# Kernel optimization log

Hardware: AMD Instinct MI355X
Metric: run time of the kernel (lower is better)

Reference implementation:

```python
import jax, jax.numpy as jnp
import numpy as np

B, N, D, H, DH = 4, 1024, 1024, 16, 64
INNER = H * DH  # 1024


def setup_inputs() -> dict:
    key = jax.random.key(0)
    k0, k1, k2, k3 = jax.random.split(key, 4)
    x = jax.random.normal(k0, (B, N, D), dtype=jnp.float32)
    # float 0/1 padding mask per token
    mask = jax.random.randint(k1, (B, N), 0, 2).astype(jnp.float32)
    w_qkv = jax.random.normal(k2, (D, 3 * INNER), dtype=jnp.float32) * (D ** -0.5)
    w_out = jax.random.normal(k3, (INNER, D), dtype=jnp.float32) * (INNER ** -0.5)
    b_out = jnp.zeros((D,), dtype=jnp.float32)
    return {"x": x, "mask": mask, "w_qkv": w_qkv, "w_out": w_out, "b_out": b_out}


def reference(x, mask, w_qkv, w_out, b_out):
    scale = DH ** -0.5
    qkv = x @ w_qkv  # [B,N,3*INNER]
    q, k, v = jnp.split(qkv, 3, axis=-1)
    resh = lambda t: t.reshape(B, N, H, DH).transpose(0, 2, 1, 3)  # b h n d
    q, k, v = resh(q), resh(k), resh(v)
    dots = jnp.einsum('bhnd,bhmd->bhnm', q, k) * scale  # [B,H,N,N]
    # attn_bias = 1 - m_i*m_j; blocked where isclose(attn_bias, 1) i.e. pair ~ 0
    pair = mask[:, None, :, None] * mask[:, None, None, :]  # [B,1,N,N]
    blocked = jnp.isclose(1.0 - pair, jnp.ones_like(pair))
    dots = jnp.where(blocked, -jnp.inf, dots)
    # fully-masked-row fixup: rows that are all -inf get dots=0, attn forced to 0
    valid = jnp.any(dots != -jnp.inf, axis=-1, keepdims=True)  # [B,H,N,1]
    dots = jnp.where(valid, dots, 0.0)
    attn = jax.nn.softmax(dots, axis=-1)
    attn = jnp.where(valid, attn, 0.0)
    out = jnp.einsum('bhnm,bhmd->bhnd', attn, v)
    out = out.transpose(0, 2, 1, 3).reshape(B, N, INNER)
    return out @ w_out + b_out
```

## Files before the change

kernel.cpp:

```cpp
#include <hip/hip_runtime.h>

#define INF __builtin_inff()

typedef __attribute__((ext_vector_type(8))) short bf16x8;
typedef __attribute__((ext_vector_type(4))) short s16x4;
typedef __attribute__((ext_vector_type(4))) float f32x4;
typedef __attribute__((ext_vector_type(8))) unsigned short u16x8;
typedef __attribute__((ext_vector_type(4))) unsigned short u16x4;

#define MFMA16(a, b, c) __builtin_amdgcn_mfma_f32_16x16x32_bf16(a, b, c, 0, 0, 0)

#define ASYNC16(g, l) __builtin_amdgcn_global_load_lds( \
    (const __attribute__((address_space(1))) unsigned int*)(const void*)(g), \
    (__attribute__((address_space(3))) unsigned int*)(void*)(l), 16, 0, 0)

__device__ __forceinline__ unsigned short f2bf(float f) {
  union { float f; unsigned u; } v; v.f = f;
  unsigned r = v.u + 0x7fffu + ((v.u >> 16) & 1u);
  return (unsigned short)(r >> 16);
}

__global__ __launch_bounds__(1024) void k_scan(
    const float* __restrict__ mask, unsigned short* __restrict__ perm, int* __restrict__ nv) {
  __shared__ int wsum[16];
  __shared__ int woff[16];
  const int b = blockIdx.x, t = threadIdx.x;
  const int wid = t >> 6, lane = t & 63;
  const bool valid = (mask[b * 1024 + t] != 0.f);
  unsigned long long bal = __ballot(valid);
  int pre = __popcll(bal & ((1ull << lane) - 1ull));
  if (lane == 0) wsum[wid] = __popcll(bal);
  __syncthreads();
  if (t < 16) { int s = 0; for (int i = 0; i < t; ++i) s += wsum[i]; woff[t] = s; }
  __syncthreads();
  int p = woff[wid] + pre;
  if (valid) perm[b * 1024 + p] = (unsigned short)t;
  if (t == 1023) nv[b] = woff[15] + wsum[15];
}

__global__ __launch_bounds__(256) void k_cvtg(
    const float* __restrict__ x, const unsigned short* __restrict__ perm,
    const int* __restrict__ nvb, unsigned short* __restrict__ xc) {
  const int id = blockIdx.x;
  const int b = id >> 10, slot = id & 1023;
  const int nv = nvb[b];
  const int ce = (nv + 127) & ~127;
  if (slot >= ce) return;
  const int t = threadIdx.x;
  u16x4 o;
  if (slot < nv) {
    int tok = perm[b * 1024 + slot];
    float4 f = ((const float4*)(x + ((size_t)(b * 1024 + tok)) * 1024))[t];
    o[0] = f2bf(f.x); o[1] = f2bf(f.y); o[2] = f2bf(f.z); o[3] = f2bf(f.w);
  } else {
    o[0] = o[1] = o[2] = o[3] = 0;
  }
  ((u16x4*)(xc + ((size_t)(b * 1024 + slot)) * 1024))[t] = o;
}

__global__ __launch_bounds__(256) void k_transpose_cvt(
    const float* __restrict__ src, unsigned short* __restrict__ dst, int R, int C) {
  __shared__ float tile[32][33];
  int bc = blockIdx.x * 32;
  int br = blockIdx.y * 32;
  int tx = threadIdx.x & 31, ty = threadIdx.x >> 5;
#pragma unroll
  for (int i = 0; i < 32; i += 8)
    tile[ty + i][tx] = src[(size_t)(br + ty + i) * C + bc + tx];
  __syncthreads();
#pragma unroll
  for (int i = 0; i < 32; i += 8)
    dst[(size_t)(bc + ty + i) * R + br + tx] = f2bf(tile[tx][ty + i]);
}

__global__ __launch_bounds__(256) void k_gemm_qkv(
    const unsigned short* __restrict__ A, const unsigned short* __restrict__ Bt,
    const int* __restrict__ nvb,
    unsigned short* __restrict__ qcmp, unsigned short* __restrict__ kcmp,
    unsigned short* __restrict__ vcmp) {
  __shared__ unsigned short SH[16384];
  unsigned short* As = SH;
  unsigned short* Bs = SH + 8192;
  const int lid = blockIdx.x;
  const int xcd = lid & 7, i6 = lid >> 3;
  const int colt = xcd * 3 + (i6 % 3);
  const int rowt = i6 / 3;
  const int b = rowt >> 3, mt = rowt & 7;
  const int nv = nvb[b];
  if (mt * 128 >= nv) return;
  const int bm0 = mt * 128;
  const int bn0 = colt * 128;
  const size_t abase = ((size_t)(b * 1024 + bm0)) * 1024;
  const int t = threadIdx.x;
  const int lane = t & 63, wave = t >> 6;
  const int wm = (wave >> 1) * 64, wn = (wave & 1) * 64;
  const int lr = lane & 15, quad = lane >> 4;
  const int sw = lr & 7;
  f32x4 acc[4][4] = {};
  for (int k0 = 0; k0 < 1024; k0 += 64) {
    __syncthreads();
#pragma unroll
    for (int j = 0; j < 4; ++j) {
      int idx = t + j * 256;
      int row = idx >> 3;
      int g = (idx ^ row) & 7;
      ASYNC16(&A[abase + (size_t)row * 1024 + k0 + g * 8], &As[idx * 8]);
      ASYNC16(&Bt[((size_t)(bn0 + row)) * 1024 + k0 + g * 8], &Bs[idx * 8]);
    }
    __syncthreads();
#pragma unroll
    for (int ks = 0; ks < 2; ++ks) {
      bf16x8 af[4], bfr[4];
#pragma unroll
      for (int i = 0; i < 4; ++i)
        af[i] = *(const bf16x8*)(&As[(wm + i * 16 + lr) * 64 + (((ks * 4 + quad) ^ sw)) * 8]);
#pragma unroll
      for (int j = 0; j < 4; ++j)
        bfr[j] = *(const bf16x8*)(&Bs[(wn + j * 16 + lr) * 64 + (((ks * 4 + quad) ^ sw)) * 8]);
#pragma unroll
      for (int i = 0; i < 4; ++i)
#pragma unroll
        for (int j = 0; j < 4; ++j)
          acc[i][j] = MFMA16(af[i], bfr[j], acc[i][j]);
    }
  }
  const int sec = bn0 >> 10;
  unsigned short* dstT = (sec == 0) ? qcmp : (sec == 1) ? kcmp : vcmp;
  const int js0 = bn0 & 1023;
#pragma unroll
  for (int hh = 0; hh < 2; ++hh) {
    __syncthreads();
    if ((wave >> 1) == hh) {
#pragma unroll
      for (int i = 0; i < 4; ++i)
#pragma unroll
        for (int j = 0; j < 4; ++j)
#pragma unroll
          for (int r = 0; r < 4; ++r)
            SH[(i * 16 + quad * 4 + r) * 136 + wn + j * 16 + lr] = f2bf(acc[i][j][r]);
    }
    __syncthreads();
#pragma unroll
    for (int rr = 0; rr < 4; ++rr) {
      int lrow = (t >> 4) + rr * 16;
      int ck = t & 15;
      int slot = bm0 + hh * 64 + lrow;
      int js = js0 + ck * 8;
      int h = js >> 6, d = js & 63;
      u16x8 v = *(u16x8*)(&SH[lrow * 136 + ck * 8]);
      *(u16x8*)(&dstT[(((size_t)(b * 16 + h)) * 1024 + slot) * 64 + d]) = v;
    }
  }
}

__global__ __launch_bounds__(256) void k_vtrans(
    const unsigned short* __restrict__ vc, unsigned short* __restrict__ vt,
    const int* __restrict__ nvb) {
  __shared__ unsigned short tile[32][33];
  const int bh = blockIdx.z;
  const int s0 = blockIdx.y * 32;
  const int d0 = blockIdx.x * 32;
  const int nv = nvb[bh >> 4];
  if (s0 >= ((nv + 63) & ~63)) return;
  const int tx = threadIdx.x & 31, ty = threadIdx.x >> 5;
  const unsigned short* src = vc + ((size_t)bh << 16);
  unsigned short* dst = vt + ((size_t)bh << 16);
#pragma unroll
  for (int i = 0; i < 32; i += 8)
    tile[ty + i][tx] = src[(size_t)(s0 + ty + i) * 64 + d0 + tx];
  __syncthreads();
#pragma unroll
  for (int i = 0; i < 32; i += 8) {
    int slot = s0 + tx;
    dst[(size_t)(d0 + ty + i) * 1024 + slot] = (slot < nv) ? tile[tx][ty + i] : (unsigned short)0;
  }
}

__global__ __launch_bounds__(256) void k_padzero(
    unsigned short* __restrict__ aoc, const int* __restrict__ nvb) {
  const int b = blockIdx.x;
  const int nv = nvb[b];
  const int ce = (nv + 63) & ~63;
  for (int r = nv; r < ce; ++r)
    ((unsigned long long*)(aoc + ((size_t)(b * 1024 + r)) * 1024))[threadIdx.x] = 0ull;
}

__global__ __launch_bounds__(256, 4) void k_attn(
    const unsigned short* __restrict__ qcmp, const unsigned short* __restrict__ kcmp,
    const unsigned short* __restrict__ vtc, const int* __restrict__ nvb,
    unsigned short* __restrict__ aoc) {
  __shared__ unsigned short Ks[64 * 64];
  __shared__ unsigned short Vs[64 * 64];
  __shared__ unsigned short P[4][16 * 72];
  const int bx = blockIdx.x;
  const int bh = (bx & 7) + 8 * (bx >> 7);
  const int qcb = (bx >> 3) & 15;
  const int b = bh >> 4, h = bh & 15;
  const int nv = nvb[b];
  if (qcb * 64 >= nv) return;
  const int t = threadIdx.x;
  const int wave = t >> 6, lane = t & 63;
  const int lr = lane & 15, quad = lane >> 4;
  const int q0 = qcb * 64 + wave * 16;
  const unsigned short* qp = qcmp + ((size_t)bh << 16);
  const unsigned short* kp = kcmp + ((size_t)bh << 16);
  const unsigned short* vp = vtc + ((size_t)bh << 16);
  unsigned short* Pw = P[wave];
  bf16x8 qv0 = *(const bf16x8*)(qp + (q0 + lr) * 64 + quad * 8);
  bf16x8 qv1 = *(const bf16x8*)(qp + (q0 + lr) * 64 + 32 + quad * 8);
  float m = -INF, l = 0.f;
  f32x4 o[4] = {};
  const int sw = lr & 7;
  const int nk = (nv + 63) >> 6;
  for (int it = 0; it < nk; ++it) {
    const int kc0 = it * 64;
    __syncthreads();
#pragma unroll
    for (int ld = 0; ld < 2; ++ld) {
      int idx = t + ld * 256;
      int row = idx >> 3;
      int gch = (idx ^ row) & 7;
      ASYNC16(kp + (kc0 + row) * 64 + gch * 8, &Ks[idx * 8]);
      ASYNC16(vp + (size_t)row * 1024 + kc0 + gch * 8, &Vs[idx * 8]);
    }
    __syncthreads();
    f32x4 st[4];
#pragma unroll
    for (int tt = 0; tt < 4; ++tt) {
      int krow = tt * 16 + lr;
      bf16x8 k0 = *(const bf16x8*)(&Ks[krow * 64 + ((quad ^ sw)) * 8]);
      bf16x8 k1 = *(const bf16x8*)(&Ks[krow * 64 + (((4 + quad) ^ sw)) * 8]);
      f32x4 c = {};
      c = MFMA16(k0, qv0, c);
      c = MFMA16(k1, qv1, c);
      st[tt] = c;
    }
    float tm = -INF;
#pragma unroll
    for (int tt = 0; tt < 4; ++tt) {
#pragma unroll
      for (int r = 0; r < 4; ++r) {
        int slot = kc0 + tt * 16 + quad * 4 + r;
        float v = (slot < nv) ? st[tt][r] * 0.125f : -INF;
        st[tt][r] = v;
        tm = fmaxf(tm, v);
      }
    }
    tm = fmaxf(tm, __shfl_xor(tm, 16));
    tm = fmaxf(tm, __shfl_xor(tm, 32));
    float mn = fmaxf(m, tm);
    float alpha = __expf(m - mn);
    if (m == -INF) alpha = 1.f;
    float ps = 0.f;
#pragma unroll
    for (int tt = 0; tt < 4; ++tt) {
      s16x4 pv;
#pragma unroll
      for (int r = 0; r < 4; ++r) {
        float pe = __expf(st[tt][r] - mn);
        ps += pe;
        pv[r] = (short)f2bf(pe);
      }
      *(s16x4*)(&Pw[lr * 72 + tt * 16 + quad * 4]) = pv;
    }
    ps += __shfl_xor(ps, 16);
    ps += __shfl_xor(ps, 32);
    l = l * alpha + ps;
    m = mn;
    float ar[4];
#pragma unroll
    for (int r = 0; r < 4; ++r) ar[r] = __shfl(alpha, quad * 4 + r);
#pragma unroll
    for (int jj = 0; jj < 4; ++jj)
#pragma unroll
      for (int r = 0; r < 4; ++r) o[jj][r] *= ar[r];
#pragma unroll
    for (int sh = 0; sh < 2; ++sh) {
      bf16x8 pa = *(const bf16x8*)(&Pw[lr * 72 + sh * 32 + quad * 8]);
#pragma unroll
      for (int jj = 0; jj < 4; ++jj) {
        bf16x8 vbf = *(const bf16x8*)(&Vs[(jj * 16 + lr) * 64 + (((sh * 4 + quad) ^ sw)) * 8]);
        o[jj] = MFMA16(pa, vbf, o[jj]);
      }
    }
  }
  float inv = 1.f / l;
  float ir[4];
#pragma unroll
  for (int r = 0; r < 4; ++r) ir[r] = __shfl(inv, quad * 4 + r);
#pragma unroll
  for (int r = 0; r < 4; ++r) {
    int slot = q0 + quad * 4 + r;
    if (slot < nv) {
      size_t rowb = ((size_t)(b * 1024 + slot)) * 1024 + h * 64;
#pragma unroll
      for (int jj = 0; jj < 4; ++jj)
        aoc[rowb + jj * 16 + lr] = f2bf(o[jj][r] * ir[r]);
    }
  }
}

__global__ __launch_bounds__(256) void k_biasfill(
    const float* __restrict__ bias, float* __restrict__ out) {
  int idx = blockIdx.x * 256 + threadIdx.x;
  int row = idx >> 8, c4 = idx & 255;
  ((float4*)out)[(size_t)row * 256 + c4] = ((const float4*)bias)[c4];
}

__global__ __launch_bounds__(256) void k_gemm_out(
    const unsigned short* __restrict__ A, const unsigned short* __restrict__ Bt,
    const unsigned short* __restrict__ perm, const int* __restrict__ nvb,
    const float* __restrict__ bias, float* __restrict__ C) {
  __shared__ unsigned short SH[12288];
  unsigned short* As = SH;
  unsigned short* Bs = SH + 4096;
  const int lid = blockIdx.x;
  const int col = lid & 7;
  const int rt = lid >> 3;
  const int b = rt >> 4, mt = rt & 15;
  const int nv = nvb[b];
  if (mt * 64 >= nv) return;
  const int bm0 = mt * 64;
  const int bn0 = col * 128;
  const size_t abase = ((size_t)(b * 1024 + bm0)) * 1024;
  const int t = threadIdx.x;
  const int lane = t & 63, wave = t >> 6;
  const int wm = (wave >> 1) * 32, wn = (wave & 1) * 64;
  const int lr = lane & 15, quad = lane >> 4;
  const int sw = lr & 7;
  f32x4 acc[2][4] = {};
  for (int k0 = 0; k0 < 1024; k0 += 64) {
    __syncthreads();
#pragma unroll
    for (int j = 0; j < 2; ++j) {
      int idx = t + j * 256;
      int row = idx >> 3;
      int g = (idx ^ row) & 7;
      ASYNC16(&A[abase + (size_t)row * 1024 + k0 + g * 8], &As[idx * 8]);
    }
#pragma unroll
    for (int j = 0; j < 4; ++j) {
      int idx = t + j * 256;
      int row = idx >> 3;
      int g = (idx ^ row) & 7;
      ASYNC16(&Bt[((size_t)(bn0 + row)) * 1024 + k0 + g * 8], &Bs[idx * 8]);
    }
    __syncthreads();
#pragma unroll
    for (int ks = 0; ks < 2; ++ks) {
      bf16x8 af[2], bfr[4];
#pragma unroll
      for (int i = 0; i < 2; ++i)
        af[i] = *(const bf16x8*)(&As[(wm + i * 16 + lr) * 64 + (((ks * 4 + quad) ^ sw)) * 8]);
#pragma unroll
      for (int j = 0; j < 4; ++j)
        bfr[j] = *(const bf16x8*)(&Bs[(wn + j * 16 + lr) * 64 + (((ks * 4 + quad) ^ sw)) * 8]);
#pragma unroll
      for (int i = 0; i < 2; ++i)
#pragma unroll
        for (int j = 0; j < 4; ++j)
          acc[i][j] = MFMA16(af[i], bfr[j], acc[i][j]);
    }
  }
#pragma unroll
  for (int i = 0; i < 2; ++i)
#pragma unroll
    for (int r = 0; r < 4; ++r) {
      int slot = bm0 + wm + i * 16 + quad * 4 + r;
      if (slot < nv) {
        int tok = perm[b * 1024 + slot];
        size_t rowb = ((size_t)(b * 1024 + tok)) * 1024;
#pragma unroll
        for (int j = 0; j < 4; ++j) {
          int c = bn0 + wn + j * 16 + lr;
          C[rowb + c] = acc[i][j][r] + bias[c];
        }
      }
    }
}

extern "C" void kernel_launch(void* const* d_in, const int* in_sizes, int n_in,
                              void* d_out, int out_size, void* d_ws, size_t ws_size,
                              hipStream_t stream) {
  const float* x    = (const float*)d_in[0];
  const float* mask = (const float*)d_in[1];
  const float* wqkv = (const float*)d_in[2];
  const float* wout = (const float*)d_in[3];
  const float* bout = (const float*)d_in[4];
  float* out = (float*)d_out;
  char* ws = (char*)d_ws;
  unsigned short* xc    = (unsigned short*)(ws);
  unsigned short* vtc   = (unsigned short*)(ws);
  unsigned short* wqkvt = (unsigned short*)(ws + (size_t)( 8 << 20));
  unsigned short* woutt = (unsigned short*)(ws + (size_t)(14 << 20));
  unsigned short* qcmp  = (unsigned short*)(ws + (size_t)(16 << 20));
  unsigned short* kcmp  = (unsigned short*)(ws + (size_t)(24 << 20));
  unsigned short* vcmp  = (unsigned short*)(ws + (size_t)(32 << 20));
  unsigned short* aoc   = (unsigned short*)(ws + (size_t)(32 << 20));
  unsigned short* perm  = (unsigned short*)(ws + (size_t)(40 << 20));
  int*            nvb   = (int*)           (ws + (size_t)(40 << 20) + 8192);

  k_scan<<<4, 1024, 0, stream>>>(mask, perm, nvb);
  k_cvtg<<<4096, 256, 0, stream>>>(x, perm, nvb, xc);
  k_transpose_cvt<<<dim3(96, 32), 256, 0, stream>>>(wqkv, wqkvt, 1024, 3072);
  k_transpose_cvt<<<dim3(32, 32), 256, 0, stream>>>(wout, woutt, 1024, 1024);
  k_gemm_qkv<<<768, 256, 0, stream>>>(xc, wqkvt, nvb, qcmp, kcmp, vcmp);
  k_vtrans<<<dim3(2, 32, 64), 256, 0, stream>>>(vcmp, vtc, nvb);
  k_padzero<<<4, 256, 0, stream>>>(aoc, nvb);
  k_attn<<<1024, 256, 0, stream>>>(qcmp, kcmp, vtc, nvb, aoc);
  k_biasfill<<<4096, 256, 0, stream>>>(bout, out);
  k_gemm_out<<<512, 256, 0, stream>>>(aoc, woutt, perm, nvb, bout, out);
}
```

Baseline: 165.0 us.

## Double-buffer GEMM/attention loads, fuse V transpose, merge and trim auxiliary kernels

Adds two-stage LDS double buffering to the QKV GEMM, the attention K/V loads and the output GEMM, so the next tile's async global-to-LDS copy is issued while the current tile is computed. The V output is now written directly in transposed layout from the QKV GEMM epilogue, which removes the separate V-transpose kernel. The two weight-transpose launches are merged into one. The attention output buffer now aliases the zero-padded xc buffer, which removes the pad-zeroing kernel. The scan also records masked tokens in perm, so the bias fill writes only masked rows instead of the whole output. Doubling the shared memory lowers attention occupancy (launch bounds go from 4 to 3 blocks) and raises LDS pressure in the GEMMs.

```diff
diff --git a/kernel.cpp b/kernel.cpp
--- a/kernel.cpp
+++ b/kernel.cpp
@@ -33,9 +33,10 @@
   __syncthreads();
   if (t < 16) { int s = 0; for (int i = 0; i < t; ++i) s += wsum[i]; woff[t] = s; }
   __syncthreads();
-  int p = woff[wid] + pre;
-  if (valid) perm[b * 1024 + p] = (unsigned short)t;
-  if (t == 1023) nv[b] = woff[15] + wsum[15];
+  const int nvt = woff[15] + wsum[15];
+  const int p = woff[wid] + pre;
+  perm[b * 1024 + (valid ? p : nvt + (t - p))] = (unsigned short)t;
+  if (t == 0) nv[b] = nvt;
 }
 
 __global__ __launch_bounds__(256) void k_cvtg(
@@ -44,8 +45,7 @@
   const int id = blockIdx.x;
   const int b = id >> 10, slot = id & 1023;
   const int nv = nvb[b];
-  const int ce = (nv + 127) & ~127;
-  if (slot >= ce) return;
+  if (slot >= ((nv + 127) & ~127)) return;
   const int t = threadIdx.x;
   u16x4 o;
   if (slot < nv) {
@@ -58,12 +58,16 @@
   ((u16x4*)(xc + ((size_t)(b * 1024 + slot)) * 1024))[t] = o;
 }
 
-__global__ __launch_bounds__(256) void k_transpose_cvt(
-    const float* __restrict__ src, unsigned short* __restrict__ dst, int R, int C) {
+__global__ __launch_bounds__(256) void k_wtrans(
+    const float* __restrict__ wqkv, const float* __restrict__ wout,
+    unsigned short* __restrict__ wqkvt, unsigned short* __restrict__ woutt) {
   __shared__ float tile[32][33];
-  int bc = blockIdx.x * 32;
-  int br = blockIdx.y * 32;
-  int tx = threadIdx.x & 31, ty = threadIdx.x >> 5;
+  int id = blockIdx.x;
+  const float* src; unsigned short* dst; int C, bc, br;
+  if (id < 3072) { src = wqkv;  dst = wqkvt; C = 3072; bc = (id % 96) * 32; br = (id / 96) * 32; }
+  else { id -= 3072; src = wout; dst = woutt; C = 1024; bc = (id & 31) * 32; br = (id >> 5) * 32; }
+  const int R = 1024;
+  const int tx = threadIdx.x & 31, ty = threadIdx.x >> 5;
 #pragma unroll
   for (int i = 0; i < 32; i += 8)
     tile[ty + i][tx] = src[(size_t)(br + ty + i) * C + bc + tx];
@@ -77,10 +81,8 @@
     const unsigned short* __restrict__ A, const unsigned short* __restrict__ Bt,
     const int* __restrict__ nvb,
     unsigned short* __restrict__ qcmp, unsigned short* __restrict__ kcmp,
-    unsigned short* __restrict__ vcmp) {
-  __shared__ unsigned short SH[16384];
-  unsigned short* As = SH;
-  unsigned short* Bs = SH + 8192;
+    unsigned short* __restrict__ vt) {
+  __shared__ unsigned short SH[32768];
   const int lid = blockIdx.x;
   const int xcd = lid & 7, i6 = lid >> 3;
   const int colt = xcd * 3 + (i6 % 3);
@@ -97,8 +99,9 @@
   const int lr = lane & 15, quad = lane >> 4;
   const int sw = lr & 7;
   f32x4 acc[4][4] = {};
-  for (int k0 = 0; k0 < 1024; k0 += 64) {
-    __syncthreads();
+  auto stage = [&](int pp, int k0) {
+    unsigned short* As = SH + pp * 16384;
+    unsigned short* Bs = As + 8192;
 #pragma unroll
     for (int j = 0; j < 4; ++j) {
       int idx = t + j * 256;
@@ -107,7 +110,14 @@
       ASYNC16(&A[abase + (size_t)row * 1024 + k0 + g * 8], &As[idx * 8]);
       ASYNC16(&Bt[((size_t)(bn0 + row)) * 1024 + k0 + g * 8], &Bs[idx * 8]);
     }
+  };
+  stage(0, 0);
+  for (int it = 0; it < 16; ++it) {
+    const int pp = it & 1;
     __syncthreads();
+    if (it + 1 < 16) stage(1 - pp, (it + 1) * 64);
+    const unsigned short* As = SH + pp * 16384;
+    const unsigned short* Bs = As + 8192;
 #pragma unroll
     for (int ks = 0; ks < 2; ++ks) {
       bf16x8 af[4], bfr[4];
@@ -125,7 +135,6 @@
     }
   }
   const int sec = bn0 >> 10;
-  unsigned short* dstT = (sec == 0) ? qcmp : (sec == 1) ? kcmp : vcmp;
   const int js0 = bn0 & 1023;
 #pragma unroll
   for (int hh = 0; hh < 2; ++hh) {
@@ -140,62 +149,45 @@
             SH[(i * 16 + quad * 4 + r) * 136 + wn + j * 16 + lr] = f2bf(acc[i][j][r]);
     }
     __syncthreads();
-#pragma unroll
-    for (int rr = 0; rr < 4; ++rr) {
-      int lrow = (t >> 4) + rr * 16;
-      int ck = t & 15;
-      int slot = bm0 + hh * 64 + lrow;
-      int js = js0 + ck * 8;
-      int h = js >> 6, d = js & 63;
-      u16x8 v = *(u16x8*)(&SH[lrow * 136 + ck * 8]);
-      *(u16x8*)(&dstT[(((size_t)(b * 16 + h)) * 1024 + slot) * 64 + d]) = v;
-    }
-  }
-}
-
-__global__ __launch_bounds__(256) void k_vtrans(
-    const unsigned short* __restrict__ vc, unsigned short* __restrict__ vt,
-    const int* __restrict__ nvb) {
-  __shared__ unsigned short tile[32][33];
-  const int bh = blockIdx.z;
-  const int s0 = blockIdx.y * 32;
-  const int d0 = blockIdx.x * 32;
-  const int nv = nvb[bh >> 4];
-  if (s0 >= ((nv + 63) & ~63)) return;
-  const int tx = threadIdx.x & 31, ty = threadIdx.x >> 5;
-  const unsigned short* src = vc + ((size_t)bh << 16);
-  unsigned short* dst = vt + ((size_t)bh << 16);
-#pragma unroll
-  for (int i = 0; i < 32; i += 8)
-    tile[ty + i][tx] = src[(size_t)(s0 + ty + i) * 64 + d0 + tx];
-  __syncthreads();
-#pragma unroll
-  for (int i = 0; i < 32; i += 8) {
-    int slot = s0 + tx;
-    dst[(size_t)(d0 + ty + i) * 1024 + slot] = (slot < nv) ? tile[tx][ty + i] : (unsigned short)0;
-  }
-}
-
-__global__ __launch_bounds__(256) void k_padzero(
-    unsigned short* __restrict__ aoc, const int* __restrict__ nvb) {
-  const int b = blockIdx.x;
-  const int nv = nvb[b];
-  const int ce = (nv + 63) & ~63;
-  for (int r = nv; r < ce; ++r)
-    ((unsigned long long*)(aoc + ((size_t)(b * 1024 + r)) * 1024))[threadIdx.x] = 0ull;
-}
-
-__global__ __launch_bounds__(256, 4) void k_attn(
+    if (sec < 2) {
+      unsigned short* dstT = sec ? kcmp : qcmp;
+#pragma unroll
+      for (int rr = 0; rr < 4; ++rr) {
+        int lrow = (t >> 4) + rr * 16;
+        int ck = t & 15;
+        int slot = bm0 + hh * 64 + lrow;
+        int js = js0 + ck * 8;
+        int h = js >> 6, d = js & 63;
+        u16x8 v = *(u16x8*)(&SH[lrow * 136 + ck * 8]);
+        *(u16x8*)(&dstT[(((size_t)(b * 16 + h)) * 1024 + slot) * 64 + d]) = v;
+      }
+    } else {
+      const int c = t & 127, seg = t >> 7;
+      const int js = js0 + c, h = js >> 6, d = js & 63;
+      unsigned short* vrow =
+          &vt[(((size_t)(b * 16 + h)) * 64 + d) * 1024 + bm0 + hh * 64 + seg * 32];
+#pragma unroll
+      for (int s4 = 0; s4 < 4; ++s4) {
+        u16x8 v;
+#pragma unroll
+        for (int s = 0; s < 8; ++s) v[s] = SH[(seg * 32 + s4 * 8 + s) * 136 + c];
+        *(u16x8*)(vrow + s4 * 8) = v;
+      }
+    }
+  }
+}
+
+__global__ __launch_bounds__(256, 3) void k_attn(
     const unsigned short* __restrict__ qcmp, const unsigned short* __restrict__ kcmp,
     const unsigned short* __restrict__ vtc, const int* __restrict__ nvb,
     unsigned short* __restrict__ aoc) {
-  __shared__ unsigned short Ks[64 * 64];
-  __shared__ unsigned short Vs[64 * 64];
+  __shared__ unsigned short Ks[2][4096];
+  __shared__ unsigned short Vs[2][4096];
   __shared__ unsigned short P[4][16 * 72];
   const int bx = blockIdx.x;
   const int bh = (bx & 7) + 8 * (bx >> 7);
   const int qcb = (bx >> 3) & 15;
-  const int b = bh >> 4, h = bh & 15;
+  const int b = bh >> 4;
   const int nv = nvb[b];
   if (qcb * 64 >= nv) return;
   const int t = threadIdx.x;
@@ -212,24 +204,28 @@
   f32x4 o[4] = {};
   const int sw = lr & 7;
   const int nk = (nv + 63) >> 6;
-  for (int it = 0; it < nk; ++it) {
-    const int kc0 = it * 64;
-    __syncthreads();
+  auto stage = [&](int pp, int kc0) {
 #pragma unroll
     for (int ld = 0; ld < 2; ++ld) {
       int idx = t + ld * 256;
       int row = idx >> 3;
-      int gch = (idx ^ row) & 7;
-      ASYNC16(kp + (kc0 + row) * 64 + gch * 8, &Ks[idx * 8]);
-      ASYNC16(vp + (size_t)row * 1024 + kc0 + gch * 8, &Vs[idx * 8]);
-    }
+      int g = (idx ^ row) & 7;
+      ASYNC16(kp + (kc0 + row) * 64 + g * 8, &Ks[pp][idx * 8]);
+      ASYNC16(vp + (size_t)row * 1024 + kc0 + g * 8, &Vs[pp][idx * 8]);
+    }
+  };
+  stage(0, 0);
+  for (int it = 0; it < nk; ++it) {
+    const int pp = it & 1;
+    const int kc0 = it * 64;
     __syncthreads();
+    if (it + 1 < nk) stage(1 - pp, kc0 + 64);
     f32x4 st[4];
 #pragma unroll
     for (int tt = 0; tt < 4; ++tt) {
       int krow = tt * 16 + lr;
-      bf16x8 k0 = *(const bf16x8*)(&Ks[krow * 64 + ((quad ^ sw)) * 8]);
-      bf16x8 k1 = *(const bf16x8*)(&Ks[krow * 64 + (((4 + quad) ^ sw)) * 8]);
+      bf16x8 k0 = *(const bf16x8*)(&Ks[pp][krow * 64 + ((quad ^ sw)) * 8]);
+      bf16x8 k1 = *(const bf16x8*)(&Ks[pp][krow * 64 + (((4 + quad) ^ sw)) * 8]);
       f32x4 c = {};
       c = MFMA16(k0, qv0, c);
       c = MFMA16(k1, qv1, c);
@@ -279,7 +275,7 @@
       bf16x8 pa = *(const bf16x8*)(&Pw[lr * 72 + sh * 32 + quad * 8]);
 #pragma unroll
       for (int jj = 0; jj < 4; ++jj) {
-        bf16x8 vbf = *(const bf16x8*)(&Vs[(jj * 16 + lr) * 64 + (((sh * 4 + quad) ^ sw)) * 8]);
+        bf16x8 vbf = *(const bf16x8*)(&Vs[pp][(jj * 16 + lr) * 64 + (((sh * 4 + quad) ^ sw)) * 8]);
         o[jj] = MFMA16(pa, vbf, o[jj]);
       }
     }
@@ -288,6 +284,7 @@
   float ir[4];
 #pragma unroll
   for (int r = 0; r < 4; ++r) ir[r] = __shfl(inv, quad * 4 + r);
+  const int h = bh & 15;
 #pragma unroll
   for (int r = 0; r < 4; ++r) {
     int slot = q0 + quad * 4 + r;
@@ -301,19 +298,20 @@
 }
 
 __global__ __launch_bounds__(256) void k_biasfill(
-    const float* __restrict__ bias, float* __restrict__ out) {
-  int idx = blockIdx.x * 256 + threadIdx.x;
-  int row = idx >> 8, c4 = idx & 255;
-  ((float4*)out)[(size_t)row * 256 + c4] = ((const float4*)bias)[c4];
+    const float* __restrict__ bias, const unsigned short* __restrict__ perm,
+    const int* __restrict__ nvb, float* __restrict__ out) {
+  const int b = blockIdx.x >> 10, slot = blockIdx.x & 1023;
+  if (slot < nvb[b]) return;
+  const int tok = perm[b * 1024 + slot];
+  ((float4*)(out + ((size_t)(b * 1024 + tok)) * 1024))[threadIdx.x] =
+      ((const float4*)bias)[threadIdx.x];
 }
 
 __global__ __launch_bounds__(256) void k_gemm_out(
     const unsigned short* __restrict__ A, const unsigned short* __restrict__ Bt,
     const unsigned short* __restrict__ perm, const int* __restrict__ nvb,
     const float* __restrict__ bias, float* __restrict__ C) {
-  __shared__ unsigned short SH[12288];
-  unsigned short* As = SH;
-  unsigned short* Bs = SH + 4096;
+  __shared__ unsigned short SH[24576];
   const int lid = blockIdx.x;
   const int col = lid & 7;
   const int rt = lid >> 3;
@@ -329,8 +327,9 @@
   const int lr = lane & 15, quad = lane >> 4;
   const int sw = lr & 7;
   f32x4 acc[2][4] = {};
-  for (int k0 = 0; k0 < 1024; k0 += 64) {
-    __syncthreads();
+  auto stage = [&](int pp, int k0) {
+    unsigned short* As = SH + pp * 12288;
+    unsigned short* Bs = As + 4096;
 #pragma unroll
     for (int j = 0; j < 2; ++j) {
       int idx = t + j * 256;
@@ -345,7 +344,14 @@
       int g = (idx ^ row) & 7;
       ASYNC16(&Bt[((size_t)(bn0 + row)) * 1024 + k0 + g * 8], &Bs[idx * 8]);
     }
+  };
+  stage(0, 0);
+  for (int it = 0; it < 16; ++it) {
+    const int pp = it & 1;
     __syncthreads();
+    if (it + 1 < 16) stage(1 - pp, (it + 1) * 64);
+    const unsigned short* As = SH + pp * 12288;
+    const unsigned short* Bs = As + 4096;
 #pragma unroll
     for (int ks = 0; ks < 2; ++ks) {
       bf16x8 af[2], bfr[4];
@@ -390,24 +396,20 @@
   float* out = (float*)d_out;
   char* ws = (char*)d_ws;
   unsigned short* xc    = (unsigned short*)(ws);
-  unsigned short* vtc   = (unsigned short*)(ws);
+  unsigned short* aoc   = (unsigned short*)(ws);
   unsigned short* wqkvt = (unsigned short*)(ws + (size_t)( 8 << 20));
   unsigned short* woutt = (unsigned short*)(ws + (size_t)(14 << 20));
   unsigned short* qcmp  = (unsigned short*)(ws + (size_t)(16 << 20));
   unsigned short* kcmp  = (unsigned short*)(ws + (size_t)(24 << 20));
-  unsigned short* vcmp  = (unsigned short*)(ws + (size_t)(32 << 20));
-  unsigned short* aoc   = (unsigned short*)(ws + (size_t)(32 << 20));
+  unsigned short* vt    = (unsigned short*)(ws + (size_t)(32 << 20));
   unsigned short* perm  = (unsigned short*)(ws + (size_t)(40 << 20));
   int*            nvb   = (int*)           (ws + (size_t)(40 << 20) + 8192);
 
   k_scan<<<4, 1024, 0, stream>>>(mask, perm, nvb);
   k_cvtg<<<4096, 256, 0, stream>>>(x, perm, nvb, xc);
-  k_transpose_cvt<<<dim3(96, 32), 256, 0, stream>>>(wqkv, wqkvt, 1024, 3072);
-  k_transpose_cvt<<<dim3(32, 32), 256, 0, stream>>>(wout, woutt, 1024, 1024);
-  k_gemm_qkv<<<768, 256, 0, stream>>>(xc, wqkvt, nvb, qcmp, kcmp, vcmp);
-  k_vtrans<<<dim3(2, 32, 64), 256, 0, stream>>>(vcmp, vtc, nvb);
-  k_padzero<<<4, 256, 0, stream>>>(aoc, nvb);
-  k_attn<<<1024, 256, 0, stream>>>(qcmp, kcmp, vtc, nvb, aoc);
-  k_biasfill<<<4096, 256, 0, stream>>>(bout, out);
+  k_wtrans<<<4096, 256, 0, stream>>>(wqkv, wout, wqkvt, woutt);
+  k_gemm_qkv<<<768, 256, 0, stream>>>(xc, wqkvt, nvb, qcmp, kcmp, vt);
+  k_attn<<<1024, 256, 0, stream>>>(qcmp, kcmp, vt, nvb, aoc);
+  k_biasfill<<<4096, 256, 0, stream>>>(bout, perm, nvb, out);
   k_gemm_out<<<512, 256, 0, stream>>>(aoc, woutt, perm, nvb, bout, out);
 }
```

Result: faster. 149.1 us (-9.6%).
